# Performance work log

Measured on AMD Instinct MI355X. Metric: run time of the kernel, lower is better.

## Reference

```python
import jax, jax.numpy as jnp
import numpy as np

N_NODES = 100000
N_EDGES = 1000000
NODE_DIM = 128
LR_VOCAB = 2000
LR_EMBED = 32
HIDDEN = 128
IN_DIM = NODE_DIM * 4 + 1 + LR_EMBED  # 545


def setup_inputs() -> dict:
    key = jax.random.key(0)
    ks = jax.random.split(key, 10)
    z = jax.random.normal(ks[0], (N_NODES, NODE_DIM), dtype=jnp.float32)
    edge_index = jax.random.randint(ks[1], (2, N_EDGES), 0, N_NODES, dtype=jnp.int64)
    # edge_attr7: col 0 = dist (float in [0,1)), col 2 = lr_id (int-valued float in [0, LR_VOCAB))
    ea = jax.random.uniform(ks[2], (N_EDGES, 7), dtype=jnp.float32)
    lr_ids = jax.random.randint(ks[3], (N_EDGES,), 0, LR_VOCAB).astype(jnp.float32)
    edge_attr7 = ea.at[:, 2].set(lr_ids)
    lr_emb = jax.random.normal(ks[4], (LR_VOCAB, LR_EMBED), dtype=jnp.float32) * 0.02
    W1 = jax.random.normal(ks[5], (IN_DIM, HIDDEN), dtype=jnp.float32) * 0.02
    b1 = jnp.zeros((HIDDEN,), dtype=jnp.float32)
    W2 = jax.random.normal(ks[6], (HIDDEN, HIDDEN), dtype=jnp.float32) * 0.02
    b2 = jnp.zeros((HIDDEN,), dtype=jnp.float32)
    W3 = jax.random.normal(ks[7], (HIDDEN, 1), dtype=jnp.float32) * 0.02
    b3 = jnp.zeros((1,), dtype=jnp.float32)
    return {"z": z, "edge_index": edge_index, "edge_attr7": edge_attr7,
            "lr_emb": lr_emb, "W1": W1, "b1": b1, "W2": W2, "b2": b2,
            "W3": W3, "b3": b3}


def reference(z, edge_index, edge_attr7, lr_emb, W1, b1, W2, b2, W3, b3):
    src = edge_index[0]
    dst = edge_index[1]
    zs = z[src]                      # [E, D]
    zd = z[dst]                      # [E, D]
    dist = edge_attr7[:, 0:1]        # [E, 1]
    lr_id = edge_attr7[:, 2].astype(jnp.int32)
    lr_vec = lr_emb[lr_id]           # [E, LR_EMBED]
    x = jnp.concatenate([zs, zd, zs * zd, jnp.abs(zs - zd), dist, lr_vec], axis=1)  # [E, IN_DIM]
    h = jax.nn.relu(x @ W1 + b1)     # dropout is identity at inference
    h = jax.nn.relu(h @ W2 + b2)
    logit = (h @ W3 + b3).reshape(-1)  # [E]
    return logit
```

## Files before the change

### kernel.cpp

```cpp
#include <hip/hip_runtime.h>

#define N_EDGES 1000000
#define HID 128
#define ME 64
#define NK1 35

typedef unsigned short ushort;
typedef unsigned int uint;
typedef __attribute__((ext_vector_type(8))) short short8;
typedef __attribute__((ext_vector_type(16))) float f32x16;

__device__ __forceinline__ float blo(uint u) { return __builtin_bit_cast(float, u << 16); }
__device__ __forceinline__ float bhi(uint u) { return __builtin_bit_cast(float, u & 0xffff0000u); }
__device__ __forceinline__ ushort f2bfbits(float f) {
  uint u = __builtin_bit_cast(uint, f);
  return (ushort)((u + 0x7fffu + ((u >> 16) & 1u)) >> 16);
}
__device__ __forceinline__ uint cvtpk(float a, float b) {
  uint r;
  asm("v_cvt_pk_bf16_f32 %0, %1, %2" : "=v"(r) : "v"(a), "v"(b));
  return r;
}
__device__ __forceinline__ uint cvtpk_abs(float a, float b) {
  uint r;
  asm("v_cvt_pk_bf16_f32 %0, abs(%1), abs(%2)" : "=v"(r) : "v"(a), "v"(b));
  return r;
}
__device__ __forceinline__ ushort bf1(float a) { return (ushort)cvtpk(a, a); }
__device__ __forceinline__ int sidx(int r, int c) {
  return r * 128 + (c ^ ((r & 7) << 3));
}

__global__ void prep_kernel(const float* __restrict__ W1, const float* __restrict__ W2,
                            ushort* __restrict__ W1p, ushort* __restrict__ W2p) {
  const int t = blockIdx.x * blockDim.x + threadIdx.x;
  const int n1 = NK1 << 11;
  if (t < n1) {
    const int j = t & 7, lane = (t >> 3) & 63, nt = (t >> 9) & 3, ks = t >> 11;
    const int col = nt * 32 + (lane & 31);
    const int kk = (lane >> 5) * 8 + j;
    float val = 0.f;
    if (ks < 32) {
      val = W1[(ks * 16 + kk) * HID + col];
    } else {
      const int c = (ks - 32) * 16 + kk;
      const int k = (c == 0) ? 512 : ((c >= 2 && c < 34) ? (511 + c) : -1);
      if (k >= 0) val = W1[k * HID + col];
    }
    W1p[t] = f2bfbits(val);
  } else {
    const int t2 = t - n1;
    if (t2 < (8 << 11)) {
      const int j = t2 & 7, lane = (t2 >> 3) & 63, nt = (t2 >> 9) & 3, ks = t2 >> 11;
      W2p[t2] = f2bfbits(W2[(ks * 16 + (lane >> 5) * 8 + j) * HID + nt * 32 + (lane & 31)]);
    }
  }
}

__global__ __launch_bounds__(256, 4)
void edge_mlp(const float* __restrict__ z, const int* __restrict__ ei,
              const float* __restrict__ ea, const float* __restrict__ lre,
              const ushort* __restrict__ W1p, const float* __restrict__ b1,
              const ushort* __restrict__ W2p, const float* __restrict__ b2,
              const float* __restrict__ W3, const float* __restrict__ b3,
              float* __restrict__ out) {
  __shared__ ushort B0[ME * 128];
  __shared__ ushort B1[ME * 128];

  const int tid = threadIdx.x;
  const int lane = tid & 63;
  const int w = tid >> 6;
  const int r15 = lane & 15;
  const int g = lane >> 4;
  const int half = lane >> 5;
  const int li = lane & 31;
  const int hi = lane >> 5;
  const int row0 = w * 16;
  const int cw = w * 32;
  const int eb = blockIdx.x * ME;

  int sd = 0;
  float auxv = 0.f;
  if (lane < 16)      sd = ei[eb + row0 + lane];
  else if (lane < 32) sd = ei[N_EDGES + eb + row0 + (lane - 16)];
  else if (lane < 48) auxv = ea[(eb + row0 + (lane - 32)) * 7 + 0];
  else                auxv = ea[(eb + row0 + (lane - 48)) * 7 + 2];

  uint2 pr_pk[8], ad_pk[8];
#pragma unroll
  for (int t = 0; t < 8; ++t) {
    const int e = 2 * t + half;
    const int r = row0 + e;
    const int s = __shfl(sd, e);
    const int d = __shfl(sd, 16 + e);
    const float4 a = *(const float4*)(z + s * HID + 4 * li);
    const float4 b = *(const float4*)(z + d * HID + 4 * li);
    uint2 zs, zd;
    zs.x = cvtpk(a.x, a.y); zs.y = cvtpk(a.z, a.w);
    zd.x = cvtpk(b.x, b.y); zd.y = cvtpk(b.z, b.w);
    *(uint2*)&B0[sidx(r, 4 * li)] = zs;
    *(uint2*)&B1[sidx(r, 4 * li)] = zd;
    pr_pk[t].x = cvtpk(a.x * b.x, a.y * b.y);
    pr_pk[t].y = cvtpk(a.z * b.z, a.w * b.w);
    ad_pk[t].x = cvtpk_abs(a.x - b.x, a.y - b.y);
    ad_pk[t].y = cvtpk_abs(a.z - b.z, a.w - b.w);
  }
  __syncthreads();

  f32x16 acc[2];
#pragma unroll
  for (int mt = 0; mt < 2; ++mt)
#pragma unroll
    for (int rg = 0; rg < 16; ++rg) acc[mt][rg] = 0.f;

#define MFMA_KS(BUF, WP, NKS, KS0)                                                      \
  _Pragma("unroll")                                                                     \
  for (int ks = 0; ks < (NKS); ++ks) {                                                  \
    const int ksg = (KS0) + ks;                                                         \
    short8 bfr = *(const short8*)((WP) + (((ksg * 4 + w) * 64) + lane) * 8);            \
    _Pragma("unroll")                                                                   \
    for (int mt = 0; mt < 2; ++mt) {                                                    \
      short8 af = *(const short8*)&BUF[sidx(mt * 32 + li, ((ksg & 7) * 16) + hi * 8)];  \
      acc[mt] = __builtin_amdgcn_mfma_f32_32x32x16_bf16(af, bfr, acc[mt], 0, 0, 0);     \
    }                                                                                   \
  }

  __builtin_amdgcn_s_setprio(1);
  MFMA_KS(B0, W1p, 8, 0)
  __builtin_amdgcn_s_setprio(0);
  __syncthreads();

#pragma unroll
  for (int t = 0; t < 8; ++t)
    *(uint2*)&B0[sidx(row0 + 2 * t + half, 4 * li)] = pr_pk[t];
  __builtin_amdgcn_s_setprio(1);
  MFMA_KS(B1, W1p, 8, 8)
  __builtin_amdgcn_s_setprio(0);
  __syncthreads();

#pragma unroll
  for (int t = 0; t < 8; ++t)
    *(uint2*)&B1[sidx(row0 + 2 * t + half, 4 * li)] = ad_pk[t];
  __builtin_amdgcn_s_setprio(1);
  MFMA_KS(B0, W1p, 8, 16)
  __builtin_amdgcn_s_setprio(0);
  __syncthreads();

  {
    const float dv = __shfl(auxv, 32 + r15);
    if (lane < 16) B0[sidx(row0 + lane, 0)] = bf1(dv);
  }
#pragma unroll
  for (int t = 0; t < 4; ++t) {
    const int e = 4 * t + g;
    const int lrid = (int)__shfl(auxv, 48 + e);
    const float2 lv = *(const float2*)(lre + lrid * 32 + 2 * r15);
    *(uint*)&B0[sidx(row0 + e, 2 + 2 * r15)] = cvtpk(lv.x, lv.y);
  }
  __builtin_amdgcn_s_setprio(1);
  MFMA_KS(B1, W1p, 8, 24)
  __builtin_amdgcn_s_setprio(0);
  __syncthreads();

  __builtin_amdgcn_s_setprio(1);
  MFMA_KS(B0, W1p, 3, 32)
  __builtin_amdgcn_s_setprio(0);
  {
    const float b1v = b1[cw + li];
#pragma unroll
    for (int mt = 0; mt < 2; ++mt)
#pragma unroll
      for (int rg = 0; rg < 16; ++rg) {
        const int row = mt * 32 + (rg & 3) + 8 * (rg >> 2) + 4 * hi;
        const float h = fmaxf(acc[mt][rg] + b1v, 0.f);
        B1[sidx(row, cw + li)] = bf1(h);
      }
  }
  __syncthreads();

#pragma unroll
  for (int mt = 0; mt < 2; ++mt)
#pragma unroll
    for (int rg = 0; rg < 16; ++rg) acc[mt][rg] = 0.f;
  __builtin_amdgcn_s_setprio(1);
  MFMA_KS(B1, W2p, 8, 0)
  __builtin_amdgcn_s_setprio(0);
  {
    const float b2v = b2[cw + li];
#pragma unroll
    for (int mt = 0; mt < 2; ++mt)
#pragma unroll
      for (int rg = 0; rg < 16; ++rg) {
        const int row = mt * 32 + (rg & 3) + 8 * (rg >> 2) + 4 * hi;
        const float h = fmaxf(acc[mt][rg] + b2v, 0.f);
        B0[sidx(row, cw + li)] = bf1(h);
      }
  }
  __syncthreads();

  {
    const int rr = w * 16 + r15;
    float sum = 0.f;
#pragma unroll
    for (int i = 0; i < 4; ++i) {
      const int c0 = g * 32 + i * 8;
      const uint4 hv = *(const uint4*)&B0[sidx(rr, c0)];
#pragma unroll
      for (int p = 0; p < 4; ++p) {
        const uint u = ((const uint*)&hv)[p];
        const float2 wv = *(const float2*)(W3 + c0 + 2 * p);
        sum += blo(u) * wv.x + bhi(u) * wv.y;
      }
    }
    sum += __shfl_xor(sum, 16);
    sum += __shfl_xor(sum, 32);
    if (lane < 16) out[eb + rr] = sum + b3[0];
  }
}

extern "C" void kernel_launch(void* const* d_in, const int* in_sizes, int n_in,
                              void* d_out, int out_size, void* d_ws, size_t ws_size,
                              hipStream_t stream) {
  const float* z   = (const float*)d_in[0];
  const int*   ei  = (const int*)d_in[1];
  const float* ea  = (const float*)d_in[2];
  const float* lre = (const float*)d_in[3];
  const float* W1  = (const float*)d_in[4];
  const float* b1  = (const float*)d_in[5];
  const float* W2  = (const float*)d_in[6];
  const float* b2  = (const float*)d_in[7];
  const float* W3  = (const float*)d_in[8];
  const float* b3  = (const float*)d_in[9];
  float* out = (float*)d_out;

  ushort* W1p = (ushort*)d_ws;
  ushort* W2p = W1p + (NK1 << 11);

  prep_kernel<<<344, 256, 0, stream>>>(W1, W2, W1p, W2p);
  edge_mlp<<<N_EDGES / ME, 256, 0, stream>>>(z, ei, ea, lre, W1p, b1, W2p, b2, W3, b3, out);
}
```

Before: 260.5 us.

## Pre-convert node features to bf16 and prefetch first weight fragment per stage

A new pre-pass converts the node feature table z to bf16 in workspace, so the edge kernel gathers 256 bytes per node row instead of 512 and copies it straight into LDS. The elementwise product and absolute difference are now computed from the bf16-rounded values. The first W1/W2 fragment of each MFMA stage is also loaded ahead of the barrier to hide its latency. The cost is one extra full pass over z on every call and slightly different numerics, and the old fp32 gather path is kept as a fallback when the workspace is too small.

```diff
diff --git a/kernel.cpp b/kernel.cpp
--- a/kernel.cpp
+++ b/kernel.cpp
@@ -1,6 +1,7 @@
 #include <hip/hip_runtime.h>
 
 #define N_EDGES 1000000
+#define N_NODES 100000
 #define HID 128
 #define ME 64
 #define NK1 35
@@ -57,8 +58,21 @@
   }
 }
 
+__global__ void prep_z(const float* __restrict__ z, ushort* __restrict__ zb) {
+  const int i = blockIdx.x * blockDim.x + threadIdx.x;
+  if (i < N_NODES * (HID / 4)) {
+    const float4 v = ((const float4*)z)[i];
+    uint2 o;
+    o.x = cvtpk(v.x, v.y);
+    o.y = cvtpk(v.z, v.w);
+    ((uint2*)zb)[i] = o;
+  }
+}
+
+template <int ZBF>
 __global__ __launch_bounds__(256, 4)
-void edge_mlp(const float* __restrict__ z, const int* __restrict__ ei,
+void edge_mlp(const float* __restrict__ z, const ushort* __restrict__ zb,
+              const int* __restrict__ ei,
               const float* __restrict__ ea, const float* __restrict__ lre,
               const ushort* __restrict__ W1p, const float* __restrict__ b1,
               const ushort* __restrict__ W2p, const float* __restrict__ b2,
@@ -86,26 +100,52 @@
   else if (lane < 48) auxv = ea[(eb + row0 + (lane - 32)) * 7 + 0];
   else                auxv = ea[(eb + row0 + (lane - 48)) * 7 + 2];
 
-  uint2 pr_pk[8], ad_pk[8];
-#pragma unroll
-  for (int t = 0; t < 8; ++t) {
-    const int e = 2 * t + half;
-    const int r = row0 + e;
-    const int s = __shfl(sd, e);
-    const int d = __shfl(sd, 16 + e);
-    const float4 a = *(const float4*)(z + s * HID + 4 * li);
-    const float4 b = *(const float4*)(z + d * HID + 4 * li);
-    uint2 zs, zd;
-    zs.x = cvtpk(a.x, a.y); zs.y = cvtpk(a.z, a.w);
-    zd.x = cvtpk(b.x, b.y); zd.y = cvtpk(b.z, b.w);
-    *(uint2*)&B0[sidx(r, 4 * li)] = zs;
-    *(uint2*)&B1[sidx(r, 4 * li)] = zd;
-    pr_pk[t].x = cvtpk(a.x * b.x, a.y * b.y);
-    pr_pk[t].y = cvtpk(a.z * b.z, a.w * b.w);
-    ad_pk[t].x = cvtpk_abs(a.x - b.x, a.y - b.y);
-    ad_pk[t].y = cvtpk_abs(a.z - b.z, a.w - b.w);
-  }
-  __syncthreads();
+  uint4 pr_pk[4], ad_pk[4];
+  if constexpr (ZBF) {
+    const int q = lane >> 4;
+    const int l16 = lane & 15;
+#pragma unroll
+    for (int t = 0; t < 4; ++t) {
+      const int e = 4 * t + q;
+      const int r = row0 + e;
+      const int s = __shfl(sd, e);
+      const int d = __shfl(sd, 16 + e);
+      const uint4 a = *(const uint4*)(zb + s * HID + 8 * l16);
+      const uint4 b = *(const uint4*)(zb + d * HID + 8 * l16);
+      *(uint4*)&B0[sidx(r, 8 * l16)] = a;
+      *(uint4*)&B1[sidx(r, 8 * l16)] = b;
+      uint4 pr, ad;
+      pr.x = cvtpk(blo(a.x) * blo(b.x), bhi(a.x) * bhi(b.x));
+      pr.y = cvtpk(blo(a.y) * blo(b.y), bhi(a.y) * bhi(b.y));
+      pr.z = cvtpk(blo(a.z) * blo(b.z), bhi(a.z) * bhi(b.z));
+      pr.w = cvtpk(blo(a.w) * blo(b.w), bhi(a.w) * bhi(b.w));
+      ad.x = cvtpk_abs(blo(a.x) - blo(b.x), bhi(a.x) - bhi(b.x));
+      ad.y = cvtpk_abs(blo(a.y) - blo(b.y), bhi(a.y) - bhi(b.y));
+      ad.z = cvtpk_abs(blo(a.z) - blo(b.z), bhi(a.z) - bhi(b.z));
+      ad.w = cvtpk_abs(blo(a.w) - blo(b.w), bhi(a.w) - bhi(b.w));
+      pr_pk[t] = pr;
+      ad_pk[t] = ad;
+    }
+  } else {
+#pragma unroll
+    for (int t = 0; t < 8; ++t) {
+      const int e = 2 * t + half;
+      const int r = row0 + e;
+      const int s = __shfl(sd, e);
+      const int d = __shfl(sd, 16 + e);
+      const float4 a = *(const float4*)(z + s * HID + 4 * li);
+      const float4 b = *(const float4*)(z + d * HID + 4 * li);
+      uint2 zs, zd;
+      zs.x = cvtpk(a.x, a.y); zs.y = cvtpk(a.z, a.w);
+      zd.x = cvtpk(b.x, b.y); zd.y = cvtpk(b.z, b.w);
+      *(uint2*)&B0[sidx(r, 4 * li)] = zs;
+      *(uint2*)&B1[sidx(r, 4 * li)] = zd;
+      ((uint2*)pr_pk)[t].x = cvtpk(a.x * b.x, a.y * b.y);
+      ((uint2*)pr_pk)[t].y = cvtpk(a.z * b.z, a.w * b.w);
+      ((uint2*)ad_pk)[t].x = cvtpk_abs(a.x - b.x, a.y - b.y);
+      ((uint2*)ad_pk)[t].y = cvtpk_abs(a.z - b.z, a.w - b.w);
+    }
+  }
 
   f32x16 acc[2];
 #pragma unroll
@@ -113,11 +153,13 @@
 #pragma unroll
     for (int rg = 0; rg < 16; ++rg) acc[mt][rg] = 0.f;
 
-#define MFMA_KS(BUF, WP, NKS, KS0)                                                      \
+#define WFRAG(WP, KSG) (*(const short8*)((WP) + ((((KSG) * 4 + w) * 64) + lane) * 8))
+
+#define MFMA_KS(BUF, WP, NKS, KS0, PF)                                                  \
   _Pragma("unroll")                                                                     \
   for (int ks = 0; ks < (NKS); ++ks) {                                                  \
     const int ksg = (KS0) + ks;                                                         \
-    short8 bfr = *(const short8*)((WP) + (((ksg * 4 + w) * 64) + lane) * 8);            \
+    short8 bfr = (ks == 0) ? (PF) : WFRAG(WP, ksg);                                     \
     _Pragma("unroll")                                                                   \
     for (int mt = 0; mt < 2; ++mt) {                                                    \
       short8 af = *(const short8*)&BUF[sidx(mt * 32 + li, ((ksg & 7) * 16) + hi * 8)];  \
@@ -125,25 +167,43 @@
     }                                                                                   \
   }
 
-  __builtin_amdgcn_s_setprio(1);
-  MFMA_KS(B0, W1p, 8, 0)
-  __builtin_amdgcn_s_setprio(0);
-  __syncthreads();
-
-#pragma unroll
-  for (int t = 0; t < 8; ++t)
-    *(uint2*)&B0[sidx(row0 + 2 * t + half, 4 * li)] = pr_pk[t];
-  __builtin_amdgcn_s_setprio(1);
-  MFMA_KS(B1, W1p, 8, 8)
-  __builtin_amdgcn_s_setprio(0);
-  __syncthreads();
-
-#pragma unroll
-  for (int t = 0; t < 8; ++t)
-    *(uint2*)&B1[sidx(row0 + 2 * t + half, 4 * li)] = ad_pk[t];
-  __builtin_amdgcn_s_setprio(1);
-  MFMA_KS(B0, W1p, 8, 16)
-  __builtin_amdgcn_s_setprio(0);
+  short8 pf = WFRAG(W1p, 0);
+  __syncthreads();
+
+  __builtin_amdgcn_s_setprio(1);
+  MFMA_KS(B0, W1p, 8, 0, pf)
+  __builtin_amdgcn_s_setprio(0);
+  pf = WFRAG(W1p, 8);
+  __syncthreads();
+
+  if constexpr (ZBF) {
+#pragma unroll
+    for (int t = 0; t < 4; ++t)
+      *(uint4*)&B0[sidx(row0 + 4 * t + (lane >> 4), 8 * (lane & 15))] = pr_pk[t];
+  } else {
+#pragma unroll
+    for (int t = 0; t < 8; ++t)
+      *(uint2*)&B0[sidx(row0 + 2 * t + half, 4 * li)] = ((uint2*)pr_pk)[t];
+  }
+  __builtin_amdgcn_s_setprio(1);
+  MFMA_KS(B1, W1p, 8, 8, pf)
+  __builtin_amdgcn_s_setprio(0);
+  pf = WFRAG(W1p, 16);
+  __syncthreads();
+
+  if constexpr (ZBF) {
+#pragma unroll
+    for (int t = 0; t < 4; ++t)
+      *(uint4*)&B1[sidx(row0 + 4 * t + (lane >> 4), 8 * (lane & 15))] = ad_pk[t];
+  } else {
+#pragma unroll
+    for (int t = 0; t < 8; ++t)
+      *(uint2*)&B1[sidx(row0 + 2 * t + half, 4 * li)] = ((uint2*)ad_pk)[t];
+  }
+  __builtin_amdgcn_s_setprio(1);
+  MFMA_KS(B0, W1p, 8, 16, pf)
+  __builtin_amdgcn_s_setprio(0);
+  pf = WFRAG(W1p, 24);
   __syncthreads();
 
   {
@@ -158,13 +218,15 @@
     *(uint*)&B0[sidx(row0 + e, 2 + 2 * r15)] = cvtpk(lv.x, lv.y);
   }
   __builtin_amdgcn_s_setprio(1);
-  MFMA_KS(B1, W1p, 8, 24)
-  __builtin_amdgcn_s_setprio(0);
-  __syncthreads();
-
-  __builtin_amdgcn_s_setprio(1);
-  MFMA_KS(B0, W1p, 3, 32)
-  __builtin_amdgcn_s_setprio(0);
+  MFMA_KS(B1, W1p, 8, 24, pf)
+  __builtin_amdgcn_s_setprio(0);
+  pf = WFRAG(W1p, 32);
+  __syncthreads();
+
+  __builtin_amdgcn_s_setprio(1);
+  MFMA_KS(B0, W1p, 3, 32, pf)
+  __builtin_amdgcn_s_setprio(0);
+  pf = WFRAG(W2p, 0);
   {
     const float b1v = b1[cw + li];
 #pragma unroll
@@ -183,7 +245,7 @@
 #pragma unroll
     for (int rg = 0; rg < 16; ++rg) acc[mt][rg] = 0.f;
   __builtin_amdgcn_s_setprio(1);
-  MFMA_KS(B1, W2p, 8, 0)
+  MFMA_KS(B1, W2p, 8, 0, pf)
   __builtin_amdgcn_s_setprio(0);
   {
     const float b2v = b2[cw + li];
@@ -235,7 +297,14 @@
 
   ushort* W1p = (ushort*)d_ws;
   ushort* W2p = W1p + (NK1 << 11);
+  ushort* zb  = W2p + (8 << 11);
+  const size_t need = (size_t)((NK1 << 11) + (8 << 11)) * 2 + (size_t)N_NODES * HID * 2;
 
   prep_kernel<<<344, 256, 0, stream>>>(W1, W2, W1p, W2p);
-  edge_mlp<<<N_EDGES / ME, 256, 0, stream>>>(z, ei, ea, lre, W1p, b1, W2p, b2, W3, b3, out);
-}
+  if (ws_size >= need) {
+    prep_z<<<(N_NODES * (HID / 4) + 255) / 256, 256, 0, stream>>>(z, zb);
+    edge_mlp<1><<<N_EDGES / ME, 256, 0, stream>>>(z, zb, ei, ea, lre, W1p, b1, W2p, b2, W3, b3, out);
+  } else {
+    edge_mlp<0><<<N_EDGES / ME, 256, 0, stream>>>(z, zb, ei, ea, lre, W1p, b1, W2p, b2, W3, b3, out);
+  }
+}
```

After: 249.7 us. 1.04x faster.
